# Performance work log

Hardware: AMD Instinct MI355X
Metric: run time of the kernel (lower is better)

The kernel has to match this reference:

```python
import jax, jax.numpy as jnp
import numpy as np

D, H, DK = 512, 8, 64
SCALE = 1.5 / 1.0  # gamma/tau, schedule='const'
NEG = -1e30


def _cross(x_q, x_kv, mask_kv, Wq, Wk, Wv, scale):
    # x_q: [B,Tq,D], x_kv: [B,Tk,D], mask_kv: [B,Tk] (1=keep, 0=mask)
    B, Tq, _ = x_q.shape
    Tk = x_kv.shape[1]
    q = (x_q @ Wq.T).reshape(B, Tq, H, DK).transpose(0, 2, 1, 3)
    k = (x_kv @ Wk.T).reshape(B, Tk, H, DK).transpose(0, 2, 1, 3)
    v = (x_kv @ Wv.T).reshape(B, Tk, H, DK).transpose(0, 2, 1, 3)
    logits = jnp.einsum('bhqd,bhkd->bhqk', q, k) * (scale / jnp.sqrt(jnp.float32(DK)))
    if mask_kv is not None:
        logits = jnp.where(mask_kv[:, None, None, :] == 0, NEG, logits)
    attn = jax.nn.softmax(logits, axis=-1)
    out = jnp.einsum('bhqk,bhkd->bhqd', attn, v)
    return out.transpose(0, 2, 1, 3).reshape(B, Tq, D)


def setup_inputs() -> dict:
    key = jax.random.key(0)
    ks = jax.random.split(key, 12)
    B, T = 4, 2048
    inp = {
        'skel_seq': jax.random.normal(ks[0], (B, T, D), jnp.float32),
        'sens_seq': jax.random.normal(ks[1], (B, T, D), jnp.float32),
        'mask_skel': jax.random.randint(ks[2], (B, T), 0, 2, jnp.int32),
        'mask_sens': jax.random.randint(ks[3], (B, T), 0, 2, jnp.int32),
    }
    s = 1.0 / np.sqrt(D)
    names = ['Wq_s2e', 'Wk_e', 'Wv_e', 'Wq_e2s', 'Wk_s', 'Wv_s', 'Wo_s', 'Wo_e']
    for i, n in enumerate(names):
        inp[n] = jax.random.normal(ks[4 + i], (D, D), jnp.float32) * s
    return inp


def reference(skel_seq, sens_seq, mask_skel, mask_sens,
              Wq_s2e, Wk_e, Wv_e, Wq_e2s, Wk_s, Wv_s, Wo_s, Wo_e):
    # skel queries attend over sensor keys/values
    s2e = _cross(skel_seq, sens_seq, mask_sens, Wq_s2e, Wk_e, Wv_e, SCALE) @ Wo_e.T
    # sensor queries attend over skeleton keys/values
    e2s = _cross(sens_seq, skel_seq, mask_skel, Wq_e2s, Wk_s, Wv_s, SCALE) @ Wo_s.T
    return (e2s, s2e)
```

## Files before the change

kernel.cpp:

```cpp
#include <hip/hip_runtime.h>
#include <hip/hip_bf16.h>

#define T_SEQ 2048
#define N_TOK 4194304
#define W_ELEM 262144


typedef float f32x4  __attribute__((ext_vector_type(4)));
typedef short bf16x8 __attribute__((ext_vector_type(8)));

#define SCALE_Q 0.27050532f

__device__ __forceinline__ unsigned short f2b(float f) {
    __hip_bfloat16 h = __float2bfloat16(f);
    return *reinterpret_cast<unsigned short*>(&h);
}

__device__ __forceinline__ int pack2bf(float lo, float hi) {
    return ((int)f2b(hi) << 16) | (int)f2b(lo);
}

__device__ __forceinline__ bf16x8 ldg8(const unsigned short* p) {
    union { int4 i; bf16x8 b; } u;
    u.i = *reinterpret_cast<const int4*>(p);
    return u.b;
}

__device__ __forceinline__ float fexp2(float x) {
#if __has_builtin(__builtin_amdgcn_exp2f)
    return __builtin_amdgcn_exp2f(x);
#else
    return exp2f(x);
#endif
}

typedef unsigned int u32_g __attribute__((address_space(1)));
typedef unsigned int u32_l __attribute__((address_space(3)));
__device__ __forceinline__ void gload_lds16(const void* g, void* l) {
    __builtin_amdgcn_global_load_lds((const u32_g*)g, (u32_l*)l, 16, 0, 0);
}

__device__ __forceinline__ void raw_barrier() {
    __builtin_amdgcn_sched_barrier(0);
    __builtin_amdgcn_s_barrier();
    __builtin_amdgcn_sched_barrier(0);
}

__global__ __launch_bounds__(256)
void prep_bias(const int* __restrict__ ms, const int* __restrict__ mk,
               float* __restrict__ dst)
{
    const int i = (blockIdx.x * 256 + threadIdx.x) * 8;
    const int* m = (i >> 13) ? mk : ms;
    const int rem = i & 8191;
    const int4 a = *reinterpret_cast<const int4*>(&m[rem]);
    const int4 b = *reinterpret_cast<const int4*>(&m[rem + 4]);
    float4 f0, f1;
    f0.x = a.x ? 0.0f : -3e38f; f0.y = a.y ? 0.0f : -3e38f;
    f0.z = a.z ? 0.0f : -3e38f; f0.w = a.w ? 0.0f : -3e38f;
    f1.x = b.x ? 0.0f : -3e38f; f1.y = b.y ? 0.0f : -3e38f;
    f1.z = b.z ? 0.0f : -3e38f; f1.w = b.w ? 0.0f : -3e38f;
    *reinterpret_cast<float4*>(&dst[i])     = f0;
    *reinterpret_cast<float4*>(&dst[i + 4]) = f1;
}

__global__ __launch_bounds__(256)
void to_bf16(const float* __restrict__ s0, const float* __restrict__ s1,
             const float* __restrict__ w0, const float* __restrict__ w1,
             const float* __restrict__ w2, const float* __restrict__ w3,
             const float* __restrict__ w4, const float* __restrict__ w5,
             unsigned short* __restrict__ dst)
{
    const int bid = blockIdx.x;
    int y, x;
    if (bid < 4096) { y = bid >> 11; x = bid & 2047; }
    else { const int t = bid - 4096; y = 2 + (t >> 7); x = t & 127; }
    const float* src;
    size_t off;
    switch (y) {
        case 0: src = s0; off = 0;      break;
        case 1: src = s1; off = N_TOK;  break;
        case 2: src = w0; off = 2 * (size_t)N_TOK;              break;
        case 3: src = w1; off = 2 * (size_t)N_TOK + 1 * W_ELEM; break;
        case 4: src = w2; off = 2 * (size_t)N_TOK + 2 * W_ELEM; break;
        case 5: src = w3; off = 2 * (size_t)N_TOK + 3 * W_ELEM; break;
        case 6: src = w4; off = 2 * (size_t)N_TOK + 4 * W_ELEM; break;
        default: src = w5; off = 2 * (size_t)N_TOK + 5 * W_ELEM; break;
    }
    const int idx = (x * 256 + threadIdx.x) * 8;
    const float4 a = *reinterpret_cast<const float4*>(src + idx);
    const float4 b = *reinterpret_cast<const float4*>(src + idx + 4);
    int4 o;
    o.x = pack2bf(a.x, a.y); o.y = pack2bf(a.z, a.w);
    o.z = pack2bf(b.x, b.y); o.w = pack2bf(b.z, b.w);
    *reinterpret_cast<int4*>(dst + off + idx) = o;
}

__global__ __launch_bounds__(256)
void wo_bf16(const float* __restrict__ we, const float* __restrict__ wsrc,
             unsigned short* __restrict__ dst)
{
    const int i = (blockIdx.x * 256 + threadIdx.x) * 8;
    const float* src = (i >= W_ELEM) ? wsrc : we;
    const int rem = i & (W_ELEM - 1);
    const float4 a = *reinterpret_cast<const float4*>(src + rem);
    const float4 b = *reinterpret_cast<const float4*>(src + rem + 4);
    int4 o;
    o.x = pack2bf(a.x, a.y); o.y = pack2bf(a.z, a.w);
    o.z = pack2bf(b.x, b.y); o.w = pack2bf(b.z, b.w);
    *reinterpret_cast<int4*>(dst + i) = o;
}

#define MF_SETUP                                                               \
    __shared__ short Asm[64][72];                                              \
    __shared__ short Wsm[64][72];                                              \
    const int tid  = threadIdx.x;                                              \
    const int lane = tid & 63;                                                 \
    const int w4   = tid >> 6;                                                 \
    const int nl   = lane & 15;                                                \
    const int quad = lane >> 4;                                                \
    const int n0 = blockIdx.x * 64;                                            \
    const int m0 = blockIdx.y * 64;                                            \
    const int arow = tid >> 2;                                                 \
    const int acol = (tid & 3) * 16;                                           \
    f32x4 acc[4] = {};

#define MF_WRITE_W                                                             \
    {                                                                          \
        int4 x;                                                                \
        x.x = pack2bf(wv[0].x, wv[0].y); x.y = pack2bf(wv[0].z, wv[0].w);      \
        x.z = pack2bf(wv[1].x, wv[1].y); x.w = pack2bf(wv[1].z, wv[1].w);      \
        *reinterpret_cast<int4*>(&Wsm[arow][acol]) = x;                        \
        x.x = pack2bf(wv[2].x, wv[2].y); x.y = pack2bf(wv[2].z, wv[2].w);      \
        x.z = pack2bf(wv[3].x, wv[3].y); x.w = pack2bf(wv[3].z, wv[3].w);      \
        *reinterpret_cast<int4*>(&Wsm[arow][acol + 8]) = x;                    \
    }

#define MF_MMA_LOOP                                                            \
    _Pragma("unroll")                                                          \
    for (int kc = 0; kc < 2; ++kc) {                                           \
        const bf16x8 a = *reinterpret_cast<const bf16x8*>(                     \
            &Asm[w4 * 16 + nl][kc * 32 + quad * 8]);                           \
        _Pragma("unroll")                                                      \
        for (int c = 0; c < 4; ++c) {                                          \
            const bf16x8 bf = *reinterpret_cast<const bf16x8*>(                \
                &Wsm[c * 16 + nl][kc * 32 + quad * 8]);                        \
            acc[c] = __builtin_amdgcn_mfma_f32_16x16x32_bf16(a, bf, acc[c],    \
                                                             0, 0, 0);         \
        }                                                                      \
    }

#define MF_CWRITE_PROJ                                                         \
    if (!trans) {                                                              \
        _Pragma("unroll")                                                      \
        for (int c = 0; c < 4; ++c)                                            \
            _Pragma("unroll")                                                  \
            for (int r = 0; r < 4; ++r)                                        \
                C[(size_t)(m0 + w4 * 16 + quad * 4 + r) * 512 + n0 + c * 16 + nl] = \
                    f2b(acc[c][r] * alpha);                                    \
    } else {                                                                   \
        const int b  = m0 >> 11;                                               \
        const int t0 = (m0 & 2047) + w4 * 16 + quad * 4;                       \
        _Pragma("unroll")                                                      \
        for (int c = 0; c < 4; ++c) {                                          \
            const int n = n0 + c * 16 + nl;                                    \
            ushort4 o;                                                         \
            o.x = f2b(acc[c][0]);                                              \
            o.y = f2b(acc[c][1]);                                              \
            o.z = f2b(acc[c][2]);                                              \
            o.w = f2b(acc[c][3]);                                              \
            *reinterpret_cast<ushort4*>(C + (size_t)(b * 512 + n) * T_SEQ + t0) = o; \
        }                                                                      \
    }

__global__ __launch_bounds__(256)
void proj_all(const float* __restrict__ skel, const float* __restrict__ sens,
              const float* __restrict__ Wq1, const float* __restrict__ Wk1,
              const float* __restrict__ Wv1, const float* __restrict__ Wq2,
              const float* __restrict__ Wk2, const float* __restrict__ Wv2,
              unsigned short* __restrict__ Q1, unsigned short* __restrict__ K1,
              unsigned short* __restrict__ Vt1, unsigned short* __restrict__ Q2,
              unsigned short* __restrict__ K2, unsigned short* __restrict__ Vt2,
              int zbase)
{
    const int z = zbase + blockIdx.z;
    const float* A; const float* W; unsigned short* C;
    float alpha = 1.0f; bool trans = false;
    switch (z) {
        case 0:  A = skel; W = Wq1; C = Q1; alpha = SCALE_Q; break;
        case 1:  A = sens; W = Wk1; C = K1; break;
        case 2:  A = sens; W = Wv1; C = Vt1; trans = true; break;
        case 3:  A = sens; W = Wq2; C = Q2; alpha = SCALE_Q; break;
        case 4:  A = skel; W = Wk2; C = K2; break;
        default: A = skel; W = Wv2; C = Vt2; trans = true; break;
    }

    MF_SETUP
    const float* ap = A + (size_t)(m0 + arow) * 512 + acol;
    const float* wp = W + (size_t)(n0 + arow) * 512 + acol;
    float4 av[4], wv[4];
    #pragma unroll
    for (int j = 0; j < 4; ++j) {
        av[j] = *reinterpret_cast<const float4*>(ap + 4 * j);
        wv[j] = *reinterpret_cast<const float4*>(wp + 4 * j);
    }
    for (int it = 0; it < 8; ++it) {
        __syncthreads();
        {
            int4 x;
            x.x = pack2bf(av[0].x, av[0].y); x.y = pack2bf(av[0].z, av[0].w);
            x.z = pack2bf(av[1].x, av[1].y); x.w = pack2bf(av[1].z, av[1].w);
            *reinterpret_cast<int4*>(&Asm[arow][acol]) = x;
            x.x = pack2bf(av[2].x, av[2].y); x.y = pack2bf(av[2].z, av[2].w);
            x.z = pack2bf(av[3].x, av[3].y); x.w = pack2bf(av[3].z, av[3].w);
            *reinterpret_cast<int4*>(&Asm[arow][acol + 8]) = x;
        }
        MF_WRITE_W
        __syncthreads();
        if (it < 7) {
            const float* apn = ap + (it + 1) * 64;
            const float* wpn = wp + (it + 1) * 64;
            #pragma unroll
            for (int j = 0; j < 4; ++j) {
                av[j] = *reinterpret_cast<const float4*>(apn + 4 * j);
                wv[j] = *reinterpret_cast<const float4*>(wpn + 4 * j);
            }
        }
        MF_MMA_LOOP
    }
    MF_CWRITE_PROJ
}

__global__ __launch_bounds__(256, 3)
void proj_fused(const unsigned short* __restrict__ skb,
                const unsigned short* __restrict__ snb,
                const unsigned short* __restrict__ wball,
                unsigned short* __restrict__ Q1, unsigned short* __restrict__ K1,
                unsigned short* __restrict__ Vt1, unsigned short* __restrict__ Q2,
                unsigned short* __restrict__ K2, unsigned short* __restrict__ Vt2)
{
    __shared__ __align__(16) char smem[49152];
    short (*Al)[128][32] = reinterpret_cast<short (*)[128][32]>(smem);
    short (*Wl)[128][32] = reinterpret_cast<short (*)[128][32]>(smem + 24576);

    const int o   = blockIdx.x;
    const int wg  = (o & 7) * 192 + (o >> 3);
    const int z   = wg >> 8;
    const int idx = wg & 255;
    const int nh  = idx & 3;
    const int mt  = idx >> 2;

    const unsigned short* A = (z == 0 || z >= 4) ? skb : snb;
    const unsigned short* W = wball + (size_t)z * W_ELEM;
    unsigned short* C;
    switch (z) {
        case 0: C = Q1;  break;
        case 1: C = K1;  break;
        case 2: C = Vt1; break;
        case 3: C = Q2;  break;
        case 4: C = K2;  break;
        default: C = Vt2; break;
    }
    const bool trans = (z == 2 || z == 5);
    const float alpha = (z == 0 || z == 3) ? SCALE_Q : 1.0f;

    const int tid  = threadIdx.x;
    const int w    = tid >> 6;
    const int wr   = w >> 1;
    const int wc   = w & 1;
    const int lane = tid & 63;
    const int nl   = lane & 15;
    const int quad = lane >> 4;
    const int rof  = lane >> 2;
    const int cg   = (lane & 3) ^ ((lane >> 3) & 3);

    const int m0g = mt * 128;
    const int n0  = nh * 128;

    const unsigned short* srcA0 = A + (size_t)(m0g + w * 32 + rof) * 512 + cg * 8;
    const unsigned short* srcA1 = srcA0 + (size_t)16 * 512;
    const unsigned short* srcW0 = W + (size_t)(n0 + w * 32 + rof) * 512 + cg * 8;
    const unsigned short* srcW1 = srcW0 + (size_t)16 * 512;

    f32x4 acc[4][4] = {};

    auto stage = [&](int it, int buf) {
        const int k0 = it * 32;
        gload_lds16(srcA0 + k0, &Al[buf][w * 32][0]);
        gload_lds16(srcA1 + k0, &Al[buf][w * 32 + 16][0]);
        gload_lds16(srcW0 + k0, &Wl[buf][w * 32][0]);
        gload_lds16(srcW1 + k0, &Wl[buf][w * 32 + 16][0]);
    };

    stage(0, 0);
    stage(1, 1);
    asm volatile("s_waitcnt vmcnt(4)" ::: "memory");
    raw_barrier();

    const int key = (nl >> 1) & 3;
    int bcur = 0, bpre = 2;
    for (int it = 0; it < 16; ++it) {
        if (it < 14) stage(it + 2, bpre);
        bf16x8 a[4], bb[4];
        #pragma unroll
        for (int am = 0; am < 4; ++am)
            a[am] = *reinterpret_cast<const bf16x8*>(
                &Al[bcur][wr * 64 + am * 16 + nl][(quad ^ key) * 8]);
        #pragma unroll
        for (int bn = 0; bn < 4; ++bn)
            bb[bn] = *reinterpret_cast<const bf16x8*>(
                &Wl[bcur][wc * 64 + bn * 16 + nl][(quad ^ key) * 8]);
        #pragma unroll
        for (int am = 0; am < 4; ++am)
            #pragma unroll
            for (int bn = 0; bn < 4; ++bn)
                acc[am][bn] = __builtin_amdgcn_mfma_f32_16x16x32_bf16(
                    a[am], bb[bn], acc[am][bn], 0, 0, 0);
        if (it < 14)       asm volatile("s_waitcnt vmcnt(4)" ::: "memory");
        else if (it == 14) asm volatile("s_waitcnt vmcnt(0)" ::: "memory");
        raw_barrier();
        bcur = (bcur == 2) ? 0 : bcur + 1;
        bpre = (bpre == 2) ? 0 : bpre + 1;
    }

    if (!trans) {
        short (*Cl)[136] = reinterpret_cast<short (*)[136]>(smem);
        #pragma unroll
        for (int am = 0; am < 4; ++am)
            #pragma unroll
            for (int bn = 0; bn < 4; ++bn)
                #pragma unroll
                for (int r = 0; r < 4; ++r)
                    Cl[wr * 64 + am * 16 + quad * 4 + r][wc * 64 + bn * 16 + nl] =
                        (short)f2b(acc[am][bn][r] * alpha);
        __syncthreads();
        const int lr = tid >> 1;
        const int ch = (tid & 1) * 64;
        unsigned short* cp = C + (size_t)(m0g + lr) * 512 + n0 + ch;
        #pragma unroll
        for (int j = 0; j < 8; ++j)
            *reinterpret_cast<int4*>(cp + j * 8) =
                *reinterpret_cast<const int4*>(&Cl[lr][ch + j * 8]);
    } else {
        short (*Tl)[136] = reinterpret_cast<short (*)[136]>(smem);
        #pragma unroll
        for (int am = 0; am < 4; ++am)
            #pragma unroll
            for (int bn = 0; bn < 4; ++bn) {
                int* dst = reinterpret_cast<int*>(
                    &Tl[wc * 64 + bn * 16 + nl][wr * 64 + am * 16 + quad * 4]);
                dst[0] = pack2bf(acc[am][bn][0], acc[am][bn][1]);
                dst[1] = pack2bf(acc[am][bn][2], acc[am][bn][3]);
            }
        __syncthreads();
        const int bq = m0g >> 11;
        const int t0 = m0g & 2047;
        const int nr = tid >> 1;
        const int tc = (tid & 1) * 64;
        unsigned short* vp = C + (size_t)(bq * 512 + n0 + nr) * T_SEQ + t0 + tc;
        #pragma unroll
        for (int j = 0; j < 8; ++j)
            *reinterpret_cast<int4*>(vp + j * 8) =
                *reinterpret_cast<const int4*>(&Tl[nr][tc + j * 8]);
    }
}

__global__ __launch_bounds__(256, 3)
void out_fused(const unsigned short* __restrict__ AO1,
               const unsigned short* __restrict__ Wb1, float* __restrict__ C1,
               const unsigned short* __restrict__ AO2,
               const unsigned short* __restrict__ Wb2, float* __restrict__ C2)
{
    __shared__ __align__(16) char smem[49152];
    short (*Al)[128][32] = reinterpret_cast<short (*)[128][32]>(smem);
    short (*Wl)[128][32] = reinterpret_cast<short (*)[128][32]>(smem + 24576);

    const int o   = blockIdx.x;
    const int wg  = (o & 7) * 64 + (o >> 3);
    const int z   = wg >> 8;
    const int idx = wg & 255;
    const int nh  = idx & 3;
    const int mt  = idx >> 2;

    const unsigned short* A = z ? AO2 : AO1;
    const unsigned short* W = z ? Wb2 : Wb1;
    float* C = z ? C2 : C1;

    const int tid  = threadIdx.x;
    const int w    = tid >> 6;
    const int wr   = w >> 1;
    const int wc   = w & 1;
    const int lane = tid & 63;
    const int nl   = lane & 15;
    const int quad = lane >> 4;
    const int rof  = lane >> 2;
    const int cg   = (lane & 3) ^ ((lane >> 3) & 3);

    const int m0g = mt * 128;
    const int n0  = nh * 128;

    const unsigned short* srcA0 = A + (size_t)(m0g + w * 32 + rof) * 512 + cg * 8;
    const unsigned short* srcA1 = srcA0 + (size_t)16 * 512;
    const unsigned short* srcW0 = W + (size_t)(n0 + w * 32 + rof) * 512 + cg * 8;
    const unsigned short* srcW1 = srcW0 + (size_t)16 * 512;

    f32x4 acc[4][4] = {};

    auto stage = [&](int it, int buf) {
        const int k0 = it * 32;
        gload_lds16(srcA0 + k0, &Al[buf][w * 32][0]);
        gload_lds16(srcA1 + k0, &Al[buf][w * 32 + 16][0]);
        gload_lds16(srcW0 + k0, &Wl[buf][w * 32][0]);
        gload_lds16(srcW1 + k0, &Wl[buf][w * 32 + 16][0]);
    };

    stage(0, 0);
    stage(1, 1);
    asm volatile("s_waitcnt vmcnt(4)" ::: "memory");
    raw_barrier();

    const int key = (nl >> 1) & 3;
    int bcur = 0, bpre = 2;
    for (int it = 0; it < 16; ++it) {
        if (it < 14) stage(it + 2, bpre);
        bf16x8 a[4], bb[4];
        #pragma unroll
        for (int am = 0; am < 4; ++am)
            a[am] = *reinterpret_cast<const bf16x8*>(
                &Al[bcur][wr * 64 + am * 16 + nl][(quad ^ key) * 8]);
        #pragma unroll
        for (int bn = 0; bn < 4; ++bn)
            bb[bn] = *reinterpret_cast<const bf16x8*>(
                &Wl[bcur][wc * 64 + bn * 16 + nl][(quad ^ key) * 8]);
        #pragma unroll
        for (int am = 0; am < 4; ++am)
            #pragma unroll
            for (int bn = 0; bn < 4; ++bn)
                acc[am][bn] = __builtin_amdgcn_mfma_f32_16x16x32_bf16(
                    a[am], bb[bn], acc[am][bn], 0, 0, 0);
        if (it < 14)       asm volatile("s_waitcnt vmcnt(4)" ::: "memory");
        else if (it == 14) asm volatile("s_waitcnt vmcnt(0)" ::: "memory");
        raw_barrier();
        bcur = (bcur == 2) ? 0 : bcur + 1;
        bpre = (bpre == 2) ? 0 : bpre + 1;
    }

    float (*Cl)[132] = reinterpret_cast<float (*)[132]>(smem);
    const int lr = tid >> 2;
    const int fc = (tid & 3) * 32;
    if (wr == 0) {
        #pragma unroll
        for (int am = 0; am < 4; ++am)
            #pragma unroll
            for (int bn = 0; bn < 4; ++bn)
                #pragma unroll
                for (int r = 0; r < 4; ++r)
                    Cl[am * 16 + quad * 4 + r][wc * 64 + bn * 16 + nl] =
                        acc[am][bn][r];
    }
    __syncthreads();
    {
        float* cp = C + (size_t)(m0g + lr) * 512 + n0 + fc;
        #pragma unroll
        for (int j = 0; j < 8; ++j)
            *reinterpret_cast<float4*>(cp + j * 4) =
                *reinterpret_cast<const float4*>(&Cl[lr][fc + j * 4]);
    }
    __syncthreads();
    if (wr == 1) {
        #pragma unroll
        for (int am = 0; am < 4; ++am)
            #pragma unroll
            for (int bn = 0; bn < 4; ++bn)
                #pragma unroll
                for (int r = 0; r < 4; ++r)
                    Cl[am * 16 + quad * 4 + r][wc * 64 + bn * 16 + nl] =
                        acc[am][bn][r];
    }
    __syncthreads();
    {
        float* cp = C + (size_t)(m0g + 64 + lr) * 512 + n0 + fc;
        #pragma unroll
        for (int j = 0; j < 8; ++j)
            *reinterpret_cast<float4*>(cp + j * 4) =
                *reinterpret_cast<const float4*>(&Cl[lr][fc + j * 4]);
    }
}

__global__ __launch_bounds__(256)
void out_proj(const unsigned short* __restrict__ AO1, const float* __restrict__ Wo1,
              float* __restrict__ C1,
              const unsigned short* __restrict__ AO2, const float* __restrict__ Wo2,
              float* __restrict__ C2, int zbase)
{
    const int z = zbase + blockIdx.z;
    const unsigned short* A = z ? AO2 : AO1;
    const float* W = z ? Wo2 : Wo1;
    float* C = z ? C2 : C1;

    MF_SETUP
    const unsigned short* ap = A + (size_t)(m0 + arow) * 512 + acol;
    const float* wp = W + (size_t)(n0 + arow) * 512 + acol;
    int4 ai[2];
    float4 wv[4];
    ai[0] = *reinterpret_cast<const int4*>(ap);
    ai[1] = *reinterpret_cast<const int4*>(ap + 8);
    #pragma unroll
    for (int j = 0; j < 4; ++j)
        wv[j] = *reinterpret_cast<const float4*>(wp + 4 * j);
    for (int it = 0; it < 8; ++it) {
        __syncthreads();
        *reinterpret_cast<int4*>(&Asm[arow][acol])     = ai[0];
        *reinterpret_cast<int4*>(&Asm[arow][acol + 8]) = ai[1];
        MF_WRITE_W
        __syncthreads();
        if (it < 7) {
            const unsigned short* apn = ap + (it + 1) * 64;
            const float* wpn = wp + (it + 1) * 64;
            ai[0] = *reinterpret_cast<const int4*>(apn);
            ai[1] = *reinterpret_cast<const int4*>(apn + 8);
            #pragma unroll
            for (int j = 0; j < 4; ++j)
                wv[j] = *reinterpret_cast<const float4*>(wpn + 4 * j);
        }
        MF_MMA_LOOP
    }
    #pragma unroll
    for (int c = 0; c < 4; ++c)
        #pragma unroll
        for (int r = 0; r < 4; ++r)
            C[(size_t)(m0 + w4 * 16 + quad * 4 + r) * 512 + n0 + c * 16 + nl] =
                acc[c][r];
}

__global__ __launch_bounds__(512)
void attn_mfma(const unsigned short* Q1x, const unsigned short* __restrict__ K1x,
               const unsigned short* __restrict__ V1x, const float* __restrict__ b1x,
               unsigned short* AO1x,
               const unsigned short* Q2x, const unsigned short* __restrict__ K2x,
               const unsigned short* __restrict__ V2x, const float* __restrict__ b2x,
               unsigned short* AO2x)
{
    __shared__ short Kl[3][64][64];
    __shared__ short Vl[3][64][64];
    __shared__ short Pl[8][16][64];

    const int dir = blockIdx.y >> 5;
    const unsigned short* Q  = dir ? Q2x : Q1x;
    const unsigned short* K  = dir ? K2x : K1x;
    const unsigned short* Vt = dir ? V2x : V1x;
    const float* biasD       = dir ? b2x : b1x;
    unsigned short* AO       = dir ? AO2x : AO1x;

    const int tid  = threadIdx.x;
    const int w    = tid >> 6;
    const int lane = tid & 63;
    const int nl   = lane & 15;
    const int quad = lane >> 4;
    const int qt = blockIdx.x;
    const int bh = blockIdx.y & 31;
    const int b = bh >> 3, h = bh & 7;
    const size_t tb = (size_t)b * (T_SEQ * 512);
    const float* biasB = biasD + b * T_SEQ;

    const int r8 = lane >> 3;
    const int cg = (lane & 7) ^ r8;
    const int sr = w * 8;

    auto stageKV = [&](int t, int buf) {
        gload_lds16(K + tb + (size_t)(t * 64 + sr + r8) * 512 + h * 64 + cg * 8,
                    &Kl[buf][sr][0]);
        gload_lds16(Vt + (size_t)(b * 512 + h * 64 + sr + r8) * T_SEQ +
                        (size_t)t * 64 + cg * 8,
                    &Vl[buf][sr][0]);
    };

    const unsigned short* qp = Q + tb + (size_t)(qt * 128 + w * 16 + nl) * 512 + h * 64 + quad * 8;
    const bf16x8 qb0 = ldg8(qp);
    const bf16x8 qb1 = ldg8(qp + 32);

    float l_run = 0.0f;
    f32x4 o[4] = {};

    stageKV(0, 0);
    stageKV(1, 1);
    asm volatile("s_waitcnt vmcnt(2)" ::: "memory");
    raw_barrier();

    const int swz = nl & 7;

    int bcur = 0, bpre = 2;
    for (int kt = 0; kt < 32; ++kt) {
        if (kt < 30) stageKV(kt + 2, bpre);
        short (*Kb)[64] = Kl[bcur];
        short (*Vb)[64] = Vl[bcur];

        float p[4][4];
        #pragma unroll
        for (int s = 0; s < 4; ++s) {
            const bf16x8 k0 = *reinterpret_cast<const bf16x8*>(&Kb[s * 16 + nl][(quad ^ swz) * 8]);
            const bf16x8 k1 = *reinterpret_cast<const bf16x8*>(&Kb[s * 16 + nl][((4 + quad) ^ swz) * 8]);
            const float4 bb = *reinterpret_cast<const float4*>(
                &biasB[kt * 64 + s * 16 + quad * 4]);
            f32x4 z = {bb.x, bb.y, bb.z, bb.w};
            z = __builtin_amdgcn_mfma_f32_16x16x32_bf16(k0, qb0, z, 0, 0, 0);
            z = __builtin_amdgcn_mfma_f32_16x16x32_bf16(k1, qb1, z, 0, 0, 0);
            p[s][0] = fexp2(z[0]);
            p[s][1] = fexp2(z[1]);
            p[s][2] = fexp2(z[2]);
            p[s][3] = fexp2(z[3]);
            l_run += p[s][0] + p[s][1] + p[s][2] + p[s][3];
        }

        #pragma unroll
        for (int s = 0; s < 4; ++s) {
            int2 pk;
            pk.x = pack2bf(p[s][0], p[s][1]);
            pk.y = pack2bf(p[s][2], p[s][3]);
            const int slot = (2 * s + (quad >> 1)) ^ swz;
            *reinterpret_cast<int2*>(&Pl[w][nl][slot * 8 + (quad & 1) * 4]) = pk;
        }

        const bf16x8 pa0 = *reinterpret_cast<const bf16x8*>(&Pl[w][nl][(quad ^ swz) * 8]);
        const bf16x8 pa1 = *reinterpret_cast<const bf16x8*>(&Pl[w][nl][((4 + quad) ^ swz) * 8]);
        __builtin_amdgcn_s_setprio(1);
        #pragma unroll
        for (int sd = 0; sd < 4; ++sd) {
            const bf16x8 v0 = *reinterpret_cast<const bf16x8*>(&Vb[sd * 16 + nl][(quad ^ swz) * 8]);
            const bf16x8 v1 = *reinterpret_cast<const bf16x8*>(&Vb[sd * 16 + nl][((4 + quad) ^ swz) * 8]);
            o[sd] = __builtin_amdgcn_mfma_f32_16x16x32_bf16(v0, pa0, o[sd], 0, 0, 0);
            o[sd] = __builtin_amdgcn_mfma_f32_16x16x32_bf16(v1, pa1, o[sd], 0, 0, 0);
        }
        __builtin_amdgcn_s_setprio(0);

        if (kt < 30)       asm volatile("s_waitcnt vmcnt(2)" ::: "memory");
        else if (kt == 30) asm volatile("s_waitcnt vmcnt(0)" ::: "memory");
        if (kt < 31) raw_barrier();
        bcur = (bcur == 2) ? 0 : bcur + 1;
        bpre = (bpre == 2) ? 0 : bpre + 1;
    }

    l_run += __shfl_xor(l_run, 16);
    l_run += __shfl_xor(l_run, 32);
    const float inv = 1.0f / l_run;
    unsigned short* ob = AO + tb + (size_t)(qt * 128 + w * 16 + nl) * 512 + h * 64 + quad * 4;
    #pragma unroll
    for (int sd = 0; sd < 4; ++sd) {
        ushort4 o4;
        o4.x = f2b(o[sd][0] * inv);
        o4.y = f2b(o[sd][1] * inv);
        o4.z = f2b(o[sd][2] * inv);
        o4.w = f2b(o[sd][3] * inv);
        *reinterpret_cast<ushort4*>(ob + sd * 16) = o4;
    }
}

extern "C" void kernel_launch(void* const* d_in, const int* in_sizes, int n_in,
                              void* d_out, int out_size, void* d_ws, size_t ws_size,
                              hipStream_t stream) {
    const float* skel = (const float*)d_in[0];
    const float* sens = (const float*)d_in[1];
    const int* mask_skel = (const int*)d_in[2];
    const int* mask_sens = (const int*)d_in[3];
    const float* Wq_s2e = (const float*)d_in[4];
    const float* Wk_e   = (const float*)d_in[5];
    const float* Wv_e   = (const float*)d_in[6];
    const float* Wq_e2s = (const float*)d_in[7];
    const float* Wk_s   = (const float*)d_in[8];
    const float* Wv_s   = (const float*)d_in[9];
    const float* Wo_s   = (const float*)d_in[10];
    const float* Wo_e   = (const float*)d_in[11];
    float* out = (float*)d_out;

    unsigned short* Q1 = (unsigned short*)d_ws;
    unsigned short* K1 = Q1 + N_TOK;
    unsigned short* V1 = K1 + N_TOK;

    const bool big = ws_size >= (size_t)6 * N_TOK * sizeof(unsigned short);

    if (big) {
        unsigned short* Q2 = V1 + N_TOK;
        unsigned short* K2 = Q2 + N_TOK;
        unsigned short* V2 = K2 + N_TOK;
        unsigned short* SC  = (unsigned short*)d_out;
        unsigned short* skb = SC;
        unsigned short* snb = SC + N_TOK;
        unsigned short* wb  = SC + 2 * (size_t)N_TOK;
        float* biasS = (float*)(SC + 2 * (size_t)N_TOK + 6 * W_ELEM);
        float* bias0 = biasS;
        float* bias1 = biasS + 4 * T_SEQ;
        prep_bias<<<dim3(8), 256, 0, stream>>>(mask_sens, mask_skel, biasS);
        to_bf16<<<dim3(4864), 256, 0, stream>>>(
            skel, sens, Wq_s2e, Wk_e, Wv_e, Wq_e2s, Wk_s, Wv_s, SC);
        proj_fused<<<dim3(1536), 256, 0, stream>>>(
            skb, snb, wb, Q1, K1, V1, Q2, K2, V2);
        attn_mfma<<<dim3(16, 64), 512, 0, stream>>>(
            Q1, K1, V1, bias0, Q1,
            Q2, K2, V2, bias1, Q2);
        wo_bf16<<<dim3(256), 256, 0, stream>>>(Wo_e, Wo_s, K1);
        out_fused<<<dim3(512), 256, 0, stream>>>(
            Q1, K1, out + N_TOK, Q2, K1 + W_ELEM, out);
    } else {
        float* bias0 = out;
        float* bias1 = out + 8192;
        prep_bias<<<dim3(8), 256, 0, stream>>>(mask_sens, mask_skel, bias0);
        proj_all<<<dim3(8, 128, 3), 256, 0, stream>>>(
            skel, sens, Wq_s2e, Wk_e, Wv_e, Wq_e2s, Wk_s, Wv_s,
            Q1, K1, V1, Q1, K1, V1, 0);
        attn_mfma<<<dim3(16, 32), 512, 0, stream>>>(
            Q1, K1, V1, bias0, Q1, Q1, K1, V1, bias0, Q1);
        out_proj<<<dim3(8, 128, 1), 256, 0, stream>>>(
            Q1, Wo_e, out + N_TOK, Q1, Wo_s, out, 0);
        proj_all<<<dim3(8, 128, 3), 256, 0, stream>>>(
            skel, sens, Wq_s2e, Wk_e, Wv_e, Wq_e2s, Wk_s, Wv_s,
            Q1, K1, V1, Q1, K1, V1, 3);
        attn_mfma<<<dim3(16, 32), 512, 0, stream>>>(
            Q1, K1, V1, bias1, Q1, Q1, K1, V1, bias1, Q1);
        out_proj<<<dim3(8, 128, 1), 256, 0, stream>>>(
            Q1, Wo_s, out, Q1, Wo_s, out, 1);
    }
}
```

Baseline: 273.6 us.

## Fold bias prep into to_bf16, remap attention grid for XCD locality, double-buffer KV

```diff
diff --git a/kernel.cpp b/kernel.cpp
--- a/kernel.cpp
+++ b/kernel.cpp
@@ -69,9 +69,25 @@
              const float* __restrict__ w0, const float* __restrict__ w1,
              const float* __restrict__ w2, const float* __restrict__ w3,
              const float* __restrict__ w4, const float* __restrict__ w5,
-             unsigned short* __restrict__ dst)
+             const int* __restrict__ ms, const int* __restrict__ mk,
+             unsigned short* __restrict__ dst, float* __restrict__ biasS)
 {
     const int bid = blockIdx.x;
+    if (bid >= 4864) {
+        const int i = ((bid - 4864) * 256 + threadIdx.x) * 8;
+        const int* m = (i >> 13) ? mk : ms;
+        const int rem = i & 8191;
+        const int4 a = *reinterpret_cast<const int4*>(&m[rem]);
+        const int4 b = *reinterpret_cast<const int4*>(&m[rem + 4]);
+        float4 f0, f1;
+        f0.x = a.x ? 0.0f : -3e38f; f0.y = a.y ? 0.0f : -3e38f;
+        f0.z = a.z ? 0.0f : -3e38f; f0.w = a.w ? 0.0f : -3e38f;
+        f1.x = b.x ? 0.0f : -3e38f; f1.y = b.y ? 0.0f : -3e38f;
+        f1.z = b.z ? 0.0f : -3e38f; f1.w = b.w ? 0.0f : -3e38f;
+        *reinterpret_cast<float4*>(&biasS[i])     = f0;
+        *reinterpret_cast<float4*>(&biasS[i + 4]) = f1;
+        return;
+    }
     int y, x;
     if (bid < 4096) { y = bid >> 11; x = bid & 2047; }
     else { const int t = bid - 4096; y = 2 + (t >> 7); x = t & 127; }
@@ -541,11 +557,18 @@
                const unsigned short* __restrict__ V2x, const float* __restrict__ b2x,
                unsigned short* AO2x)
 {
-    __shared__ short Kl[3][64][64];
-    __shared__ short Vl[3][64][64];
+    __shared__ short Kl[2][64][64];
+    __shared__ short Vl[2][64][64];
     __shared__ short Pl[8][16][64];
 
-    const int dir = blockIdx.y >> 5;
+    const int o   = blockIdx.x;
+    const int qx  = gridDim.x >> 3;
+    const int wg  = (o & 7) * qx + (o >> 3);
+    const int qt  = wg & 15;
+    const int bhd = wg >> 4;
+    const int dir = bhd >> 5;
+    const int bh  = bhd & 31;
+
     const unsigned short* Q  = dir ? Q2x : Q1x;
     const unsigned short* K  = dir ? K2x : K1x;
     const unsigned short* Vt = dir ? V2x : V1x;
@@ -557,8 +580,6 @@
     const int lane = tid & 63;
     const int nl   = lane & 15;
     const int quad = lane >> 4;
-    const int qt = blockIdx.x;
-    const int bh = blockIdx.y & 31;
     const int b = bh >> 3, h = bh & 7;
     const size_t tb = (size_t)b * (T_SEQ * 512);
     const float* biasB = biasD + b * T_SEQ;
@@ -567,33 +588,31 @@
     const int cg = (lane & 7) ^ r8;
     const int sr = w * 8;
 
-    auto stageKV = [&](int t, int buf) {
-        gload_lds16(K + tb + (size_t)(t * 64 + sr + r8) * 512 + h * 64 + cg * 8,
-                    &Kl[buf][sr][0]);
-        gload_lds16(Vt + (size_t)(b * 512 + h * 64 + sr + r8) * T_SEQ +
-                        (size_t)t * 64 + cg * 8,
-                    &Vl[buf][sr][0]);
-    };
-
     const unsigned short* qp = Q + tb + (size_t)(qt * 128 + w * 16 + nl) * 512 + h * 64 + quad * 8;
     const bf16x8 qb0 = ldg8(qp);
     const bf16x8 qb1 = ldg8(qp + 32);
 
     float l_run = 0.0f;
-    f32x4 o[4] = {};
-
-    stageKV(0, 0);
-    stageKV(1, 1);
-    asm volatile("s_waitcnt vmcnt(2)" ::: "memory");
-    raw_barrier();
+    f32x4 oacc[4] = {};
+
+    gload_lds16(K  + tb + (size_t)(sr + r8) * 512 + h * 64 + cg * 8, &Kl[0][sr][0]);
+    gload_lds16(Vt + (size_t)(b * 512 + h * 64 + sr + r8) * T_SEQ + cg * 8, &Vl[0][sr][0]);
+    asm volatile("s_waitcnt vmcnt(0)" ::: "memory");
+    __syncthreads();
 
     const int swz = nl & 7;
 
-    int bcur = 0, bpre = 2;
     for (int kt = 0; kt < 32; ++kt) {
-        if (kt < 30) stageKV(kt + 2, bpre);
-        short (*Kb)[64] = Kl[bcur];
-        short (*Vb)[64] = Vl[bcur];
+        const int cur = kt & 1;
+        short (*Kb)[64] = Kl[cur];
+        short (*Vb)[64] = Vl[cur];
+
+        if (kt < 31) {
+            short (*Kn)[64] = Kl[cur ^ 1];
+            short (*Vn)[64] = Vl[cur ^ 1];
+            gload_lds16(K  + tb + (size_t)((kt + 1) * 64 + sr + r8) * 512 + h * 64 + cg * 8, &Kn[sr][0]);
+            gload_lds16(Vt + (size_t)(b * 512 + h * 64 + sr + r8) * T_SEQ + (size_t)(kt + 1) * 64 + cg * 8, &Vn[sr][0]);
+        }
 
         float p[4][4];
         #pragma unroll
@@ -628,16 +647,13 @@
         for (int sd = 0; sd < 4; ++sd) {
             const bf16x8 v0 = *reinterpret_cast<const bf16x8*>(&Vb[sd * 16 + nl][(quad ^ swz) * 8]);
             const bf16x8 v1 = *reinterpret_cast<const bf16x8*>(&Vb[sd * 16 + nl][((4 + quad) ^ swz) * 8]);
-            o[sd] = __builtin_amdgcn_mfma_f32_16x16x32_bf16(v0, pa0, o[sd], 0, 0, 0);
-            o[sd] = __builtin_amdgcn_mfma_f32_16x16x32_bf16(v1, pa1, o[sd], 0, 0, 0);
+            oacc[sd] = __builtin_amdgcn_mfma_f32_16x16x32_bf16(v0, pa0, oacc[sd], 0, 0, 0);
+            oacc[sd] = __builtin_amdgcn_mfma_f32_16x16x32_bf16(v1, pa1, oacc[sd], 0, 0, 0);
         }
         __builtin_amdgcn_s_setprio(0);
 
-        if (kt < 30)       asm volatile("s_waitcnt vmcnt(2)" ::: "memory");
-        else if (kt == 30) asm volatile("s_waitcnt vmcnt(0)" ::: "memory");
-        if (kt < 31) raw_barrier();
-        bcur = (bcur == 2) ? 0 : bcur + 1;
-        bpre = (bpre == 2) ? 0 : bpre + 1;
+        asm volatile("s_waitcnt vmcnt(0)" ::: "memory");
+        __syncthreads();
     }
 
     l_run += __shfl_xor(l_run, 16);
@@ -646,12 +662,12 @@
     unsigned short* ob = AO + tb + (size_t)(qt * 128 + w * 16 + nl) * 512 + h * 64 + quad * 4;
     #pragma unroll
     for (int sd = 0; sd < 4; ++sd) {
-        ushort4 o4;
-        o4.x = f2b(o[sd][0] * inv);
-        o4.y = f2b(o[sd][1] * inv);
-        o4.z = f2b(o[sd][2] * inv);
-        o4.w = f2b(o[sd][3] * inv);
-        *reinterpret_cast<ushort4*>(ob + sd * 16) = o4;
+        ushort4 ov;
+        ov.x = f2b(oacc[sd][0] * inv);
+        ov.y = f2b(oacc[sd][1] * inv);
+        ov.z = f2b(oacc[sd][2] * inv);
+        ov.w = f2b(oacc[sd][3] * inv);
+        *reinterpret_cast<ushort4*>(ob + sd * 16) = ov;
     }
 }
 
@@ -689,12 +705,12 @@
         float* biasS = (float*)(SC + 2 * (size_t)N_TOK + 6 * W_ELEM);
         float* bias0 = biasS;
         float* bias1 = biasS + 4 * T_SEQ;
-        prep_bias<<<dim3(8), 256, 0, stream>>>(mask_sens, mask_skel, biasS);
-        to_bf16<<<dim3(4864), 256, 0, stream>>>(
-            skel, sens, Wq_s2e, Wk_e, Wv_e, Wq_e2s, Wk_s, Wv_s, SC);
+        to_bf16<<<dim3(4872), 256, 0, stream>>>(
+            skel, sens, Wq_s2e, Wk_e, Wv_e, Wq_e2s, Wk_s, Wv_s,
+            mask_sens, mask_skel, SC, biasS);
         proj_fused<<<dim3(1536), 256, 0, stream>>>(
             skb, snb, wb, Q1, K1, V1, Q2, K2, V2);
-        attn_mfma<<<dim3(16, 64), 512, 0, stream>>>(
+        attn_mfma<<<dim3(1024), 512, 0, stream>>>(
             Q1, K1, V1, bias0, Q1,
             Q2, K2, V2, bias1, Q2);
         wo_bf16<<<dim3(256), 256, 0, stream>>>(Wo_e, Wo_s, K1);
@@ -707,14 +723,14 @@
         proj_all<<<dim3(8, 128, 3), 256, 0, stream>>>(
             skel, sens, Wq_s2e, Wk_e, Wv_e, Wq_e2s, Wk_s, Wv_s,
             Q1, K1, V1, Q1, K1, V1, 0);
-        attn_mfma<<<dim3(16, 32), 512, 0, stream>>>(
+        attn_mfma<<<dim3(512), 512, 0, stream>>>(
             Q1, K1, V1, bias0, Q1, Q1, K1, V1, bias0, Q1);
         out_proj<<<dim3(8, 128, 1), 256, 0, stream>>>(
             Q1, Wo_e, out + N_TOK, Q1, Wo_s, out, 0);
         proj_all<<<dim3(8, 128, 3), 256, 0, stream>>>(
             skel, sens, Wq_s2e, Wk_e, Wv_e, Wq_e2s, Wk_s, Wv_s,
             Q1, K1, V1, Q1, K1, V1, 3);
-        attn_mfma<<<dim3(16, 32), 512, 0, stream>>>(
+        attn_mfma<<<dim3(512), 512, 0, stream>>>(
             Q1, K1, V1, bias1, Q1, Q1, K1, V1, bias1, Q1);
         out_proj<<<dim3(8, 128, 1), 256, 0, stream>>>(
             Q1, Wo_s, out, Q1, Wo_s, out, 1);
```

After: 264.4 us. -3.4%, faster.
